# Kernel tuning notes

Measured on AMD Instinct MI355X. Metric: run time of the kernel, lower is better.

Reference implementation:

```python
import jax, jax.numpy as jnp
import numpy as np

N_NODES = 100000
N_EDGES = 1600000
D_IN = 256
N_HEADS = 4
D_OUT = 32
NEG_SLOPE = 0.2


def setup_inputs() -> dict:
    key = jax.random.key(0)
    k1, k2, k3, k4, k5, k6 = jax.random.split(key, 6)
    x = jax.random.normal(k1, (N_NODES, D_IN), dtype=jnp.float32)
    fc_w = jax.random.normal(k2, (N_HEADS * D_OUT, D_IN), dtype=jnp.float32) * (1.0 / np.sqrt(D_IN))
    attn_l = jax.random.normal(k3, (N_HEADS, D_OUT), dtype=jnp.float32) * 0.1
    attn_r = jax.random.normal(k4, (N_HEADS, D_OUT), dtype=jnp.float32) * 0.1
    src = jax.random.randint(k5, (N_EDGES,), 0, N_NODES, dtype=jnp.int64)
    dst = jax.random.randint(k6, (N_EDGES,), 0, N_NODES, dtype=jnp.int64)
    return {"x": x, "fc_w": fc_w, "attn_l": attn_l, "attn_r": attn_r, "src": src, "dst": dst}


def reference(x, fc_w, attn_l, attn_r, src, dst):
    N = x.shape[0]
    H, F = attn_l.shape
    # Linear projection: ft = fc(x) viewed as [N, H, F]
    ft = (x @ fc_w.T).reshape(N, H, F)
    # Per-node attention logits: el = <ft, a_l>, er = <ft, a_r>  -> [N, H]
    el = jnp.einsum("nhf,hf->nh", ft, attn_l)
    er = jnp.einsum("nhf,hf->nh", ft, attn_r)
    # Edge scores: e = leaky_relu(el[src] + er[dst])  -> [E, H]
    e = el[src] + er[dst]
    e = jnp.where(e > 0, e, NEG_SLOPE * e)
    # Segment (per-destination-node) softmax over incoming edges
    m = jax.ops.segment_max(e, dst, num_segments=N)  # [N, H]
    ex = jnp.exp(e - m[dst])                          # [E, H]
    denom = jax.ops.segment_sum(ex, dst, num_segments=N)  # [N, H]
    a = ex / denom[dst]                               # [E, H]
    # Weighted scatter-sum aggregation: out[n] = sum_{e: dst=n} a_e * ft[src_e]
    out = jax.ops.segment_sum(ft[src] * a[:, :, None], dst, num_segments=N)  # [N, H, F]
    return out
```

## Files before the change

kernel.cpp:

```cpp
#include <hip/hip_runtime.h>
#include <math.h>

#define N_NODES 100000
#define N_EDGES 1600000
#define D_IN 256
#define N_HEADS 4
#define D_OUT 32
#define D_HID 128
#define NEG_SLOPE 0.2f

#define BUCKET_SHIFT 8
#define BUCKET_NODES 256
#define NB ((N_NODES + BUCKET_NODES - 1) / BUCKET_NODES)
#define CAP 6144
#define TILE 2048
#define EPT 8
#define N_TILES ((N_EDGES + TILE - 1) / TILE)

typedef __attribute__((ext_vector_type(8))) short bf16x8;
typedef __attribute__((ext_vector_type(4))) float f32x4;

static __device__ __forceinline__ unsigned cvt2(float lo, float hi) {
  unsigned r;
  asm("v_cvt_pk_bf16_f32 %0, %1, %2" : "=v"(r) : "v"(lo), "v"(hi));
  return r;
}
static __device__ __forceinline__ float bfu_lo(unsigned u) {
  union { unsigned u; float f; } c; c.u = u << 16; return c.f;
}
static __device__ __forceinline__ float bfu_hi(unsigned u) {
  union { unsigned u; float f; } c; c.u = u & 0xFFFF0000u; return c.f;
}

#define LDA 40
__global__ __launch_bounds__(256) void k_gemm(const float* __restrict__ x,
                                              const float* __restrict__ w,
                                              unsigned short* __restrict__ ftb) {
  __shared__ short As[128 * LDA];
  __shared__ short Bs[128 * LDA];
  int t = threadIdx.x;
  int wave = t >> 6, lane = t & 63;
  int quad = lane >> 4, l16 = lane & 15;
  int rowBase = blockIdx.x * 128;
  int wm = (wave >> 1) * 64, wn = (wave & 1) * 64;
  f32x4 acc[4][4];
  #pragma unroll
  for (int mt = 0; mt < 4; ++mt)
    #pragma unroll
    for (int nt = 0; nt < 4; ++nt) {
      acc[mt][nt][0] = 0.f; acc[mt][nt][1] = 0.f;
      acc[mt][nt][2] = 0.f; acc[mt][nt][3] = 0.f;
    }

  for (int kb = 0; kb < D_IN; kb += 32) {
    #pragma unroll
    for (int p = 0; p < 4; ++p) {
      int idx = p * 256 + t;
      int r = idx >> 3;
      int kq = (idx & 7) * 4;
      int row = rowBase + r;
      float4 v = make_float4(0.f, 0.f, 0.f, 0.f);
      if (row < N_NODES) v = *(const float4*)&x[(size_t)row * D_IN + kb + kq];
      unsigned* d = (unsigned*)&As[r * LDA + kq];
      d[0] = cvt2(v.x, v.y);
      d[1] = cvt2(v.z, v.w);
    }
    #pragma unroll
    for (int p = 0; p < 4; ++p) {
      int idx = p * 256 + t;
      int r = idx >> 3;
      int kq = (idx & 7) * 4;
      float4 v = *(const float4*)&w[(size_t)r * D_IN + kb + kq];
      unsigned* d = (unsigned*)&Bs[r * LDA + kq];
      d[0] = cvt2(v.x, v.y);
      d[1] = cvt2(v.z, v.w);
    }
    __syncthreads();
    bf16x8 af[4], bfr[4];
    #pragma unroll
    for (int mt = 0; mt < 4; ++mt)
      af[mt] = *(const bf16x8*)&As[(wm + mt * 16 + l16) * LDA + quad * 8];
    #pragma unroll
    for (int nt = 0; nt < 4; ++nt)
      bfr[nt] = *(const bf16x8*)&Bs[(wn + nt * 16 + l16) * LDA + quad * 8];
    #pragma unroll
    for (int mt = 0; mt < 4; ++mt)
      #pragma unroll
      for (int nt = 0; nt < 4; ++nt)
        acc[mt][nt] = __builtin_amdgcn_mfma_f32_16x16x32_bf16(af[mt], bfr[nt], acc[mt][nt], 0, 0, 0);
    __syncthreads();
  }
  #pragma unroll
  for (int mt = 0; mt < 4; ++mt) {
    #pragma unroll
    for (int nt = 0; nt < 4; ++nt) {
      int col = wn + nt * 16 + l16;
      #pragma unroll
      for (int r = 0; r < 4; r += 2) {
        unsigned p = cvt2(acc[mt][nt][r], acc[mt][nt][r + 1]);
        int row = rowBase + wm + mt * 16 + quad * 4 + r;
        if (row < N_NODES)
          ftb[(size_t)row * D_HID + col] = (unsigned short)p;
        if (row + 1 < N_NODES)
          ftb[(size_t)(row + 1) * D_HID + col] = (unsigned short)(p >> 16);
      }
    }
  }
}

__global__ void k_eler(const unsigned short* __restrict__ ftb,
                       const float* __restrict__ al,
                       const float* __restrict__ ar,
                       float* __restrict__ el, float* __restrict__ er) {
  int gid = blockIdx.x * blockDim.x + threadIdx.x;
  if (gid >= N_NODES * N_HEADS) return;
  int n = gid >> 2, h = gid & 3;
  const unsigned* f = (const unsigned*)&ftb[(size_t)n * D_HID + h * D_OUT];
  const float* alh = &al[h * D_OUT];
  const float* arh = &ar[h * D_OUT];
  float sl = 0.f, sr = 0.f;
  #pragma unroll
  for (int i = 0; i < 16; ++i) {
    unsigned u = f[i];
    float lo = bfu_lo(u), hi = bfu_hi(u);
    sl += lo * alh[2 * i] + hi * alh[2 * i + 1];
    sr += lo * arh[2 * i] + hi * arh[2 * i + 1];
  }
  el[gid] = sl;
  er[gid] = sr;
}

__global__ __launch_bounds__(256) void k_bucket(const int* __restrict__ src,
                                                const int* __restrict__ dst,
                                                int* __restrict__ gfill,
                                                unsigned* __restrict__ pairs) {
  __shared__ int bcnt[NB];
  __shared__ int brsv[NB];
  __shared__ int brank[NB];
  int t = threadIdx.x;
  for (int tile = blockIdx.x; tile < N_TILES; tile += gridDim.x) {
    int e0 = tile * TILE + t * EPT;
    for (int i = t; i < NB; i += 256) { bcnt[i] = 0; brank[i] = 0; }
    __syncthreads();
    int ds[EPT], ss[EPT];
    if (e0 + EPT <= N_EDGES) {
      *(int4*)&ds[0] = *(const int4*)&dst[e0];
      *(int4*)&ds[4] = *(const int4*)&dst[e0 + 4];
      *(int4*)&ss[0] = *(const int4*)&src[e0];
      *(int4*)&ss[4] = *(const int4*)&src[e0 + 4];
    } else {
      #pragma unroll
      for (int k = 0; k < EPT; ++k) {
        int e = e0 + k;
        ds[k] = (e < N_EDGES) ? dst[e] : -1;
        ss[k] = (e < N_EDGES) ? src[e] : 0;
      }
    }
    #pragma unroll
    for (int k = 0; k < EPT; ++k)
      if (ds[k] >= 0) atomicAdd(&bcnt[ds[k] >> BUCKET_SHIFT], 1);
    __syncthreads();
    for (int i = t; i < NB; i += 256) {
      int c = bcnt[i];
      brsv[i] = (c > 0) ? atomicAdd(&gfill[i], c) : 0;
    }
    __syncthreads();
    #pragma unroll
    for (int k = 0; k < EPT; ++k) {
      if (ds[k] >= 0) {
        int b = ds[k] >> BUCKET_SHIFT;
        int r = brsv[b] + atomicAdd(&brank[b], 1);
        if (r < CAP)
          pairs[(size_t)b * CAP + r] =
              ((unsigned)ss[k] << 8) | (unsigned)(ds[k] & (BUCKET_NODES - 1));
      }
    }
    __syncthreads();
  }
}

__global__ __launch_bounds__(512) void k_scanbuckets(const int* __restrict__ gfill,
                                                     int* __restrict__ bbase,
                                                     int* __restrict__ offs) {
  __shared__ int ss[512];
  int t = threadIdx.x;
  int v = (t < NB) ? gfill[t] : 0;
  ss[t] = v;
  __syncthreads();
  #pragma unroll
  for (int d = 1; d < 512; d <<= 1) {
    int u = (t >= d) ? ss[t - d] : 0;
    __syncthreads();
    ss[t] += u;
    __syncthreads();
  }
  if (t < NB) bbase[t] = (t == 0) ? 0 : ss[t - 1];
  if (t == 0) offs[N_NODES] = N_EDGES;
}

__global__ __launch_bounds__(512) void k_localsort(const unsigned* __restrict__ pairs,
                                                   const int* __restrict__ gfill,
                                                   const int* __restrict__ bbase,
                                                   int* __restrict__ offs,
                                                   int* __restrict__ ssrc) {
  __shared__ int cnt_l[256];
  __shared__ int ss[256];
  __shared__ int cur_l[256];
  int b = blockIdx.x, t = threadIdx.x;
  int E = min(gfill[b], CAP);
  int base = bbase[b];
  const unsigned* pb = &pairs[(size_t)b * CAP];
  if (t < 256) cnt_l[t] = 0;
  __syncthreads();
  for (int i = t; i < E; i += 512)
    atomicAdd(&cnt_l[pb[i] & (BUCKET_NODES - 1)], 1);
  __syncthreads();
  if (t < 256) ss[t] = cnt_l[t];
  __syncthreads();
  #pragma unroll
  for (int d = 1; d < 256; d <<= 1) {
    int u = (t < 256 && t >= d) ? ss[t - d] : 0;
    __syncthreads();
    if (t < 256) ss[t] += u;
    __syncthreads();
  }
  if (t < 256) {
    int pre = (t == 0) ? 0 : ss[t - 1];
    int node = b * BUCKET_NODES + t;
    if (node < N_NODES) offs[node] = base + pre;
    cur_l[t] = pre;
  }
  __syncthreads();
  for (int i = t; i < E; i += 512) {
    unsigned p = pb[i];
    int pos = atomicAdd(&cur_l[p & (BUCKET_NODES - 1)], 1);
    ssrc[base + pos] = (int)(p >> 8);
  }
}

#define AHP 72
__global__ __launch_bounds__(256) void k_agg(const int* __restrict__ offs,
                                             const int* __restrict__ ssrc,
                                             const unsigned short* __restrict__ ftb,
                                             const float* __restrict__ el,
                                             const float* __restrict__ er,
                                             float* __restrict__ out) {
  __shared__ int   lds_s[4][64];
  __shared__ float lds_ah[4][4][AHP];
  int wave = threadIdx.x >> 6;
  int lane = threadIdx.x & 63;
  int n = blockIdx.x * 4 + wave;
  if (n >= N_NODES) return;
  int start = offs[n], end = offs[n + 1];
  int deg = end - start;

  if (deg <= 64) {
    float4 er4 = *(const float4*)&er[n * 4];
    bool valid = lane < deg;
    int s = valid ? ssrc[start + lane] : 0;
    float4 e4 = *(const float4*)&el[s * 4];
    float v[4] = {e4.x + er4.x, e4.y + er4.y, e4.z + er4.z, e4.w + er4.w};
    float m[4], ex[4], den[4];
    #pragma unroll
    for (int h = 0; h < 4; ++h) {
      v[h] = v[h] > 0.f ? v[h] : NEG_SLOPE * v[h];
      m[h] = valid ? v[h] : -INFINITY;
    }
    #pragma unroll
    for (int h = 0; h < 4; ++h)
      #pragma unroll
      for (int o = 32; o > 0; o >>= 1) m[h] = fmaxf(m[h], __shfl_xor(m[h], o));
    #pragma unroll
    for (int h = 0; h < 4; ++h) {
      ex[h] = valid ? __expf(v[h] - m[h]) : 0.f;
      den[h] = ex[h];
    }
    #pragma unroll
    for (int h = 0; h < 4; ++h)
      #pragma unroll
      for (int o = 32; o > 0; o >>= 1) den[h] += __shfl_xor(den[h], o);
    lds_s[wave][lane] = s;
    #pragma unroll
    for (int h = 0; h < 4; ++h)
      lds_ah[wave][h][lane] = ex[h] / den[h];
    __builtin_amdgcn_wave_barrier();

    int epar = lane >> 5;
    int c4 = (lane & 31) * 4;
    int hh = c4 >> 5;
    const unsigned short* fb = ftb + c4;
    float acc[4] = {0.f, 0.f, 0.f, 0.f};
    for (int j = 0; j < deg; j += 8) {
      int4   sv0 = *(const int4*)&lds_s[wave][j];
      int4   sv1 = *(const int4*)&lds_s[wave][j + 4];
      float4 av0 = *(const float4*)&lds_ah[wave][hh][j];
      float4 av1 = *(const float4*)&lds_ah[wave][hh][j + 4];
      int   sA = epar ? sv0.y : sv0.x;  float aA = epar ? av0.y : av0.x;
      int   sB = epar ? sv0.w : sv0.z;  float aB = epar ? av0.w : av0.z;
      int   sC = epar ? sv1.y : sv1.x;  float aC = epar ? av1.y : av1.x;
      int   sD = epar ? sv1.w : sv1.z;  float aD = epar ? av1.w : av1.z;
      uint2 uA = *(const uint2*)&fb[(size_t)sA * D_HID];
      uint2 uB = *(const uint2*)&fb[(size_t)sB * D_HID];
      uint2 uC = *(const uint2*)&fb[(size_t)sC * D_HID];
      uint2 uD = *(const uint2*)&fb[(size_t)sD * D_HID];
      acc[0] += aA * bfu_lo(uA.x); acc[1] += aA * bfu_hi(uA.x);
      acc[2] += aA * bfu_lo(uA.y); acc[3] += aA * bfu_hi(uA.y);
      acc[0] += aB * bfu_lo(uB.x); acc[1] += aB * bfu_hi(uB.x);
      acc[2] += aB * bfu_lo(uB.y); acc[3] += aB * bfu_hi(uB.y);
      acc[0] += aC * bfu_lo(uC.x); acc[1] += aC * bfu_hi(uC.x);
      acc[2] += aC * bfu_lo(uC.y); acc[3] += aC * bfu_hi(uC.y);
      acc[0] += aD * bfu_lo(uD.x); acc[1] += aD * bfu_hi(uD.x);
      acc[2] += aD * bfu_lo(uD.y); acc[3] += aD * bfu_hi(uD.y);
    }
    #pragma unroll
    for (int i = 0; i < 4; ++i) acc[i] += __shfl_xor(acc[i], 32);
    if (epar == 0)
      *(float4*)&out[(size_t)n * D_HID + c4] =
          make_float4(acc[0], acc[1], acc[2], acc[3]);
  } else {
    int f0 = lane * 2;
    int hh = lane >> 4;
    float2 acc = {0.f, 0.f};
    float4 er4 = *(const float4*)&er[n * 4];
    float erh[4] = {er4.x, er4.y, er4.z, er4.w};
    float m[4] = {-INFINITY, -INFINITY, -INFINITY, -INFINITY};
    for (int c = start; c < end; c += 64) {
      int i = c + lane;
      bool valid = i < end;
      int s = valid ? ssrc[i] : 0;
      float4 e4 = *(const float4*)&el[s * 4];
      float ee[4] = {e4.x, e4.y, e4.z, e4.w};
      #pragma unroll
      for (int h = 0; h < 4; ++h) {
        float v = ee[h] + erh[h];
        v = v > 0.f ? v : NEG_SLOPE * v;
        if (!valid) v = -INFINITY;
        m[h] = fmaxf(m[h], v);
      }
    }
    #pragma unroll
    for (int h = 0; h < 4; ++h)
      #pragma unroll
      for (int o = 32; o > 0; o >>= 1) m[h] = fmaxf(m[h], __shfl_xor(m[h], o));
    float den[4] = {0.f, 0.f, 0.f, 0.f};
    for (int c = start; c < end; c += 64) {
      int i = c + lane;
      bool valid = i < end;
      int s = valid ? ssrc[i] : 0;
      float4 e4 = *(const float4*)&el[s * 4];
      float ee[4] = {e4.x, e4.y, e4.z, e4.w};
      #pragma unroll
      for (int h = 0; h < 4; ++h) {
        float v = ee[h] + erh[h];
        v = v > 0.f ? v : NEG_SLOPE * v;
        den[h] += valid ? __expf(v - m[h]) : 0.f;
      }
    }
    #pragma unroll
    for (int h = 0; h < 4; ++h)
      #pragma unroll
      for (int o = 32; o > 0; o >>= 1) den[h] += __shfl_xor(den[h], o);
    float invd = 1.f / den[hh];
    for (int c = start; c < end; c += 64) {
      int i = c + lane;
      bool valid = i < end;
      int s = valid ? ssrc[i] : 0;
      float4 e4 = *(const float4*)&el[s * 4];
      float ee[4] = {e4.x, e4.y, e4.z, e4.w};
      float ex[4];
      #pragma unroll
      for (int h = 0; h < 4; ++h) {
        float v = ee[h] + erh[h];
        v = v > 0.f ? v : NEG_SLOPE * v;
        ex[h] = __expf(v - m[h]);
      }
      int cnt2 = min(64, end - c);
      for (int j = 0; j < cnt2; ++j) {
        int sj = __shfl(s, j);
        float a0 = __shfl(ex[0], j);
        float a1 = __shfl(ex[1], j);
        float a2 = __shfl(ex[2], j);
        float a3 = __shfl(ex[3], j);
        float ah = hh == 0 ? a0 : (hh == 1 ? a1 : (hh == 2 ? a2 : a3));
        ah *= invd;
        unsigned u = *(const unsigned*)&ftb[(size_t)sj * D_HID + f0];
        acc.x += ah * bfu_lo(u);
        acc.y += ah * bfu_hi(u);
      }
    }
    *(float2*)&out[(size_t)n * D_HID + f0] = acc;
  }
}

extern "C" void kernel_launch(void* const* d_in, const int* in_sizes, int n_in,
                              void* d_out, int out_size, void* d_ws, size_t ws_size,
                              hipStream_t stream) {
  const float* x      = (const float*)d_in[0];
  const float* fc_w   = (const float*)d_in[1];
  const float* attn_l = (const float*)d_in[2];
  const float* attn_r = (const float*)d_in[3];
  const int*   src    = (const int*)d_in[4];
  const int*   dst    = (const int*)d_in[5];
  float* out = (float*)d_out;

  char* wsp = (char*)d_ws;
  size_t off = 0;
  auto alloc = [&](size_t bytes) {
    void* p = wsp + off;
    off = (off + bytes + 255) & ~(size_t)255;
    return p;
  };
  unsigned short* ftb = (unsigned short*)alloc((size_t)N_NODES * D_HID * 2);
  float* el     = (float*)alloc((size_t)N_NODES * 4 * 4);
  float* er     = (float*)alloc((size_t)N_NODES * 4 * 4);
  int*   offs   = (int*)alloc((size_t)(N_NODES + 1) * 4);
  int*   ssrc   = (int*)alloc((size_t)N_EDGES * 4);
  int*   gfill  = (int*)alloc((size_t)NB * 4);
  int*   bbase  = (int*)alloc((size_t)NB * 4);
  unsigned* pairs = (unsigned*)alloc((size_t)NB * CAP * 4);

  hipMemsetAsync(gfill, 0, (size_t)NB * 4, stream);
  k_gemm<<<(N_NODES + 127) / 128, 256, 0, stream>>>(x, fc_w, ftb);
  k_eler<<<(N_NODES * N_HEADS + 255) / 256, 256, 0, stream>>>(ftb, attn_l, attn_r, el, er);
  k_bucket<<<N_TILES, 256, 0, stream>>>(src, dst, gfill, pairs);
  k_scanbuckets<<<1, 512, 0, stream>>>(gfill, bbase, offs);
  k_localsort<<<NB, 512, 0, stream>>>(pairs, gfill, bbase, offs, ssrc);
  k_agg<<<(N_NODES + 3) / 4, 256, 0, stream>>>(offs, ssrc, ftb, el, er, out);
}
```

Baseline: 324.7 us.

## Fuse el/er into GEMM epilogue, fold bucket scan into localsort, half-wave aggregation

Computes the per-node attention logits el/er directly from the fp32 MFMA accumulators in the GEMM epilogue using 16-lane shuffle reductions, which removes the separate k_eler kernel and its re-read of the bf16 features. The single-block bucket scan kernel is dropped; each localsort block now sums the fill counts of the preceding buckets itself. The aggregation kernel now assigns one node per half-wave (32 lanes, 4 features each), staging neighbor ids and attention weights in LDS for both low- and high-degree paths. This cuts kernel launches and idle lanes for typical degree ~16, at the cost of more shuffles in the GEMM epilogue and redundant prefix sums across localsort blocks.

```diff
diff --git a/kernel.cpp b/kernel.cpp
--- a/kernel.cpp
+++ b/kernel.cpp
@@ -35,7 +35,11 @@
 #define LDA 40
 __global__ __launch_bounds__(256) void k_gemm(const float* __restrict__ x,
                                               const float* __restrict__ w,
-                                              unsigned short* __restrict__ ftb) {
+                                              const float* __restrict__ al,
+                                              const float* __restrict__ ar,
+                                              unsigned short* __restrict__ ftb,
+                                              float* __restrict__ el,
+                                              float* __restrict__ er) {
   __shared__ short As[128 * LDA];
   __shared__ short Bs[128 * LDA];
   int t = threadIdx.x;
@@ -90,6 +94,7 @@
         acc[mt][nt] = __builtin_amdgcn_mfma_f32_16x16x32_bf16(af[mt], bfr[nt], acc[mt][nt], 0, 0, 0);
     __syncthreads();
   }
+
   #pragma unroll
   for (int mt = 0; mt < 4; ++mt) {
     #pragma unroll
@@ -106,38 +111,48 @@
       }
     }
   }
-}
-
-__global__ void k_eler(const unsigned short* __restrict__ ftb,
-                       const float* __restrict__ al,
-                       const float* __restrict__ ar,
-                       float* __restrict__ el, float* __restrict__ er) {
-  int gid = blockIdx.x * blockDim.x + threadIdx.x;
-  if (gid >= N_NODES * N_HEADS) return;
-  int n = gid >> 2, h = gid & 3;
-  const unsigned* f = (const unsigned*)&ftb[(size_t)n * D_HID + h * D_OUT];
-  const float* alh = &al[h * D_OUT];
-  const float* arh = &ar[h * D_OUT];
-  float sl = 0.f, sr = 0.f;
+
+  float alf[4], arf[4];
   #pragma unroll
-  for (int i = 0; i < 16; ++i) {
-    unsigned u = f[i];
-    float lo = bfu_lo(u), hi = bfu_hi(u);
-    sl += lo * alh[2 * i] + hi * alh[2 * i + 1];
-    sr += lo * arh[2 * i] + hi * arh[2 * i + 1];
-  }
-  el[gid] = sl;
-  er[gid] = sr;
+  for (int q = 0; q < 4; ++q) {
+    alf[q] = al[wn + q * 16 + l16];
+    arf[q] = ar[wn + q * 16 + l16];
+  }
+  int h0 = wn >> 5;
+  #pragma unroll
+  for (int mt = 0; mt < 4; ++mt) {
+    #pragma unroll
+    for (int r = 0; r < 4; ++r) {
+      float sl0 = acc[mt][0][r] * alf[0] + acc[mt][1][r] * alf[1];
+      float sl1 = acc[mt][2][r] * alf[2] + acc[mt][3][r] * alf[3];
+      float sr0 = acc[mt][0][r] * arf[0] + acc[mt][1][r] * arf[1];
+      float sr1 = acc[mt][2][r] * arf[2] + acc[mt][3][r] * arf[3];
+      #pragma unroll
+      for (int o = 1; o < 16; o <<= 1) {
+        sl0 += __shfl_xor(sl0, o);
+        sl1 += __shfl_xor(sl1, o);
+        sr0 += __shfl_xor(sr0, o);
+        sr1 += __shfl_xor(sr1, o);
+      }
+      int row = rowBase + wm + mt * 16 + quad * 4 + r;
+      if (l16 == 0 && row < N_NODES) {
+        *(float2*)&el[row * 4 + h0] = make_float2(sl0, sl1);
+        *(float2*)&er[row * 4 + h0] = make_float2(sr0, sr1);
+      }
+    }
+  }
 }
 
 __global__ __launch_bounds__(256) void k_bucket(const int* __restrict__ src,
                                                 const int* __restrict__ dst,
                                                 int* __restrict__ gfill,
-                                                unsigned* __restrict__ pairs) {
+                                                unsigned* __restrict__ pairs,
+                                                int* __restrict__ offs) {
   __shared__ int bcnt[NB];
   __shared__ int brsv[NB];
   __shared__ int brank[NB];
   int t = threadIdx.x;
+  if (blockIdx.x == 0 && t == 0) offs[N_NODES] = N_EDGES;
   for (int tile = blockIdx.x; tile < N_TILES; tile += gridDim.x) {
     int e0 = tile * TILE + t * EPT;
     for (int i = t; i < NB; i += 256) { bcnt[i] = 0; brank[i] = 0; }
@@ -179,39 +194,34 @@
   }
 }
 
-__global__ __launch_bounds__(512) void k_scanbuckets(const int* __restrict__ gfill,
-                                                     int* __restrict__ bbase,
-                                                     int* __restrict__ offs) {
-  __shared__ int ss[512];
-  int t = threadIdx.x;
-  int v = (t < NB) ? gfill[t] : 0;
-  ss[t] = v;
-  __syncthreads();
-  #pragma unroll
-  for (int d = 1; d < 512; d <<= 1) {
-    int u = (t >= d) ? ss[t - d] : 0;
-    __syncthreads();
-    ss[t] += u;
-    __syncthreads();
-  }
-  if (t < NB) bbase[t] = (t == 0) ? 0 : ss[t - 1];
-  if (t == 0) offs[N_NODES] = N_EDGES;
-}
-
 __global__ __launch_bounds__(512) void k_localsort(const unsigned* __restrict__ pairs,
                                                    const int* __restrict__ gfill,
-                                                   const int* __restrict__ bbase,
                                                    int* __restrict__ offs,
                                                    int* __restrict__ ssrc) {
   __shared__ int cnt_l[256];
   __shared__ int ss[256];
   __shared__ int cur_l[256];
+  __shared__ int redsum[8];
+  __shared__ int s_base;
   int b = blockIdx.x, t = threadIdx.x;
-  int E = min(gfill[b], CAP);
-  int base = bbase[b];
-  const unsigned* pb = &pairs[(size_t)b * CAP];
+  {
+    int v = (t < NB && t < b) ? gfill[t] : 0;
+    #pragma unroll
+    for (int o = 32; o > 0; o >>= 1) v += __shfl_xor(v, o);
+    if ((t & 63) == 0) redsum[t >> 6] = v;
+  }
   if (t < 256) cnt_l[t] = 0;
   __syncthreads();
+  if (t == 0) {
+    int s = 0;
+    #pragma unroll
+    for (int i = 0; i < 8; ++i) s += redsum[i];
+    s_base = s;
+  }
+  int E = min(gfill[b], CAP);
+  const unsigned* pb = &pairs[(size_t)b * CAP];
+  __syncthreads();
+  int base = s_base;
   for (int i = t; i < E; i += 512)
     atomicAdd(&cnt_l[pb[i] & (BUCKET_NODES - 1)], 1);
   __syncthreads();
@@ -238,26 +248,37 @@
   }
 }
 
-#define AHP 72
+#define AH_PAD 36
 __global__ __launch_bounds__(256) void k_agg(const int* __restrict__ offs,
                                              const int* __restrict__ ssrc,
                                              const unsigned short* __restrict__ ftb,
                                              const float* __restrict__ el,
                                              const float* __restrict__ er,
                                              float* __restrict__ out) {
-  __shared__ int   lds_s[4][64];
-  __shared__ float lds_ah[4][4][AHP];
+  __shared__ int   lds_s[4][2][32];
+  __shared__ float lds_ah[4][2][4][AH_PAD];
   int wave = threadIdx.x >> 6;
   int lane = threadIdx.x & 63;
-  int n = blockIdx.x * 4 + wave;
+  int half = lane >> 5;
+  int l32 = lane & 31;
+  int n = blockIdx.x * 8 + wave * 2 + half;
   if (n >= N_NODES) return;
   int start = offs[n], end = offs[n + 1];
   int deg = end - start;
 
-  if (deg <= 64) {
-    float4 er4 = *(const float4*)&er[n * 4];
-    bool valid = lane < deg;
-    int s = valid ? ssrc[start + lane] : 0;
+  int* sS = lds_s[wave][half];
+  float (*sA)[AH_PAD] = lds_ah[wave][half];
+
+  int c4 = l32 * 4;
+  int hh = l32 >> 3;
+  const unsigned short* fb = ftb + c4;
+  float a0 = 0.f, a1 = 0.f, a2 = 0.f, a3 = 0.f;
+
+  float4 er4 = *(const float4*)&er[n * 4];
+
+  if (deg <= 32) {
+    bool valid = l32 < deg;
+    int s = valid ? ssrc[start + l32] : 0;
     float4 e4 = *(const float4*)&el[s * 4];
     float v[4] = {e4.x + er4.x, e4.y + er4.y, e4.z + er4.z, e4.w + er4.w};
     float m[4], ex[4], den[4];
@@ -269,7 +290,7 @@
     #pragma unroll
     for (int h = 0; h < 4; ++h)
       #pragma unroll
-      for (int o = 32; o > 0; o >>= 1) m[h] = fmaxf(m[h], __shfl_xor(m[h], o));
+      for (int o = 16; o > 0; o >>= 1) m[h] = fmaxf(m[h], __shfl_xor(m[h], o));
     #pragma unroll
     for (int h = 0; h < 4; ++h) {
       ex[h] = valid ? __expf(v[h] - m[h]) : 0.f;
@@ -278,54 +299,32 @@
     #pragma unroll
     for (int h = 0; h < 4; ++h)
       #pragma unroll
-      for (int o = 32; o > 0; o >>= 1) den[h] += __shfl_xor(den[h], o);
-    lds_s[wave][lane] = s;
-    #pragma unroll
-    for (int h = 0; h < 4; ++h)
-      lds_ah[wave][h][lane] = ex[h] / den[h];
+      for (int o = 16; o > 0; o >>= 1) den[h] += __shfl_xor(den[h], o);
+    sS[l32] = s;
+    #pragma unroll
+    for (int h = 0; h < 4; ++h) sA[h][l32] = ex[h] / den[h];
     __builtin_amdgcn_wave_barrier();
-
-    int epar = lane >> 5;
-    int c4 = (lane & 31) * 4;
-    int hh = c4 >> 5;
-    const unsigned short* fb = ftb + c4;
-    float acc[4] = {0.f, 0.f, 0.f, 0.f};
-    for (int j = 0; j < deg; j += 8) {
-      int4   sv0 = *(const int4*)&lds_s[wave][j];
-      int4   sv1 = *(const int4*)&lds_s[wave][j + 4];
-      float4 av0 = *(const float4*)&lds_ah[wave][hh][j];
-      float4 av1 = *(const float4*)&lds_ah[wave][hh][j + 4];
-      int   sA = epar ? sv0.y : sv0.x;  float aA = epar ? av0.y : av0.x;
-      int   sB = epar ? sv0.w : sv0.z;  float aB = epar ? av0.w : av0.z;
-      int   sC = epar ? sv1.y : sv1.x;  float aC = epar ? av1.y : av1.x;
-      int   sD = epar ? sv1.w : sv1.z;  float aD = epar ? av1.w : av1.z;
-      uint2 uA = *(const uint2*)&fb[(size_t)sA * D_HID];
-      uint2 uB = *(const uint2*)&fb[(size_t)sB * D_HID];
-      uint2 uC = *(const uint2*)&fb[(size_t)sC * D_HID];
-      uint2 uD = *(const uint2*)&fb[(size_t)sD * D_HID];
-      acc[0] += aA * bfu_lo(uA.x); acc[1] += aA * bfu_hi(uA.x);
-      acc[2] += aA * bfu_lo(uA.y); acc[3] += aA * bfu_hi(uA.y);
-      acc[0] += aB * bfu_lo(uB.x); acc[1] += aB * bfu_hi(uB.x);
-      acc[2] += aB * bfu_lo(uB.y); acc[3] += aB * bfu_hi(uB.y);
-      acc[0] += aC * bfu_lo(uC.x); acc[1] += aC * bfu_hi(uC.x);
-      acc[2] += aC * bfu_lo(uC.y); acc[3] += aC * bfu_hi(uC.y);
-      acc[0] += aD * bfu_lo(uD.x); acc[1] += aD * bfu_hi(uD.x);
-      acc[2] += aD * bfu_lo(uD.y); acc[3] += aD * bfu_hi(uD.y);
-    }
-    #pragma unroll
-    for (int i = 0; i < 4; ++i) acc[i] += __shfl_xor(acc[i], 32);
-    if (epar == 0)
-      *(float4*)&out[(size_t)n * D_HID + c4] =
-          make_float4(acc[0], acc[1], acc[2], acc[3]);
+    for (int j = 0; j < deg; j += 4) {
+      int4   sv = *(const int4*)&sS[j];
+      float4 av = *(const float4*)&sA[hh][j];
+      uint2 uA = *(const uint2*)&fb[(size_t)sv.x * D_HID];
+      uint2 uB = *(const uint2*)&fb[(size_t)sv.y * D_HID];
+      uint2 uC = *(const uint2*)&fb[(size_t)sv.z * D_HID];
+      uint2 uD = *(const uint2*)&fb[(size_t)sv.w * D_HID];
+      a0 += av.x * bfu_lo(uA.x); a1 += av.x * bfu_hi(uA.x);
+      a2 += av.x * bfu_lo(uA.y); a3 += av.x * bfu_hi(uA.y);
+      a0 += av.y * bfu_lo(uB.x); a1 += av.y * bfu_hi(uB.x);
+      a2 += av.y * bfu_lo(uB.y); a3 += av.y * bfu_hi(uB.y);
+      a0 += av.z * bfu_lo(uC.x); a1 += av.z * bfu_hi(uC.x);
+      a2 += av.z * bfu_lo(uC.y); a3 += av.z * bfu_hi(uC.y);
+      a0 += av.w * bfu_lo(uD.x); a1 += av.w * bfu_hi(uD.x);
+      a2 += av.w * bfu_lo(uD.y); a3 += av.w * bfu_hi(uD.y);
+    }
   } else {
-    int f0 = lane * 2;
-    int hh = lane >> 4;
-    float2 acc = {0.f, 0.f};
-    float4 er4 = *(const float4*)&er[n * 4];
     float erh[4] = {er4.x, er4.y, er4.z, er4.w};
     float m[4] = {-INFINITY, -INFINITY, -INFINITY, -INFINITY};
-    for (int c = start; c < end; c += 64) {
-      int i = c + lane;
+    for (int c = start; c < end; c += 32) {
+      int i = c + l32;
       bool valid = i < end;
       int s = valid ? ssrc[i] : 0;
       float4 e4 = *(const float4*)&el[s * 4];
@@ -334,17 +333,16 @@
       for (int h = 0; h < 4; ++h) {
         float v = ee[h] + erh[h];
         v = v > 0.f ? v : NEG_SLOPE * v;
-        if (!valid) v = -INFINITY;
-        m[h] = fmaxf(m[h], v);
+        m[h] = fmaxf(m[h], valid ? v : -INFINITY);
       }
     }
     #pragma unroll
     for (int h = 0; h < 4; ++h)
       #pragma unroll
-      for (int o = 32; o > 0; o >>= 1) m[h] = fmaxf(m[h], __shfl_xor(m[h], o));
+      for (int o = 16; o > 0; o >>= 1) m[h] = fmaxf(m[h], __shfl_xor(m[h], o));
     float den[4] = {0.f, 0.f, 0.f, 0.f};
-    for (int c = start; c < end; c += 64) {
-      int i = c + lane;
+    for (int c = start; c < end; c += 32) {
+      int i = c + l32;
       bool valid = i < end;
       int s = valid ? ssrc[i] : 0;
       float4 e4 = *(const float4*)&el[s * 4];
@@ -359,37 +357,48 @@
     #pragma unroll
     for (int h = 0; h < 4; ++h)
       #pragma unroll
-      for (int o = 32; o > 0; o >>= 1) den[h] += __shfl_xor(den[h], o);
-    float invd = 1.f / den[hh];
-    for (int c = start; c < end; c += 64) {
-      int i = c + lane;
+      for (int o = 16; o > 0; o >>= 1) den[h] += __shfl_xor(den[h], o);
+    float invd[4];
+    #pragma unroll
+    for (int h = 0; h < 4; ++h) invd[h] = 1.f / den[h];
+    for (int c = start; c < end; c += 32) {
+      int i = c + l32;
       bool valid = i < end;
       int s = valid ? ssrc[i] : 0;
       float4 e4 = *(const float4*)&el[s * 4];
       float ee[4] = {e4.x, e4.y, e4.z, e4.w};
-      float ex[4];
+      float av[4];
       #pragma unroll
       for (int h = 0; h < 4; ++h) {
         float v = ee[h] + erh[h];
         v = v > 0.f ? v : NEG_SLOPE * v;
-        ex[h] = __expf(v - m[h]);
-      }
-      int cnt2 = min(64, end - c);
-      for (int j = 0; j < cnt2; ++j) {
-        int sj = __shfl(s, j);
-        float a0 = __shfl(ex[0], j);
-        float a1 = __shfl(ex[1], j);
-        float a2 = __shfl(ex[2], j);
-        float a3 = __shfl(ex[3], j);
-        float ah = hh == 0 ? a0 : (hh == 1 ? a1 : (hh == 2 ? a2 : a3));
-        ah *= invd;
-        unsigned u = *(const unsigned*)&ftb[(size_t)sj * D_HID + f0];
-        acc.x += ah * bfu_lo(u);
-        acc.y += ah * bfu_hi(u);
-      }
-    }
-    *(float2*)&out[(size_t)n * D_HID + f0] = acc;
-  }
+        av[h] = valid ? __expf(v - m[h]) * invd[h] : 0.f;
+      }
+      __builtin_amdgcn_wave_barrier();
+      sS[l32] = s;
+      #pragma unroll
+      for (int h = 0; h < 4; ++h) sA[h][l32] = av[h];
+      __builtin_amdgcn_wave_barrier();
+      int cnt = min(32, end - c);
+      for (int j = 0; j < cnt; j += 4) {
+        int4   sv = *(const int4*)&sS[j];
+        float4 aw = *(const float4*)&sA[hh][j];
+        uint2 uA = *(const uint2*)&fb[(size_t)sv.x * D_HID];
+        uint2 uB = *(const uint2*)&fb[(size_t)sv.y * D_HID];
+        uint2 uC = *(const uint2*)&fb[(size_t)sv.z * D_HID];
+        uint2 uD = *(const uint2*)&fb[(size_t)sv.w * D_HID];
+        a0 += aw.x * bfu_lo(uA.x); a1 += aw.x * bfu_hi(uA.x);
+        a2 += aw.x * bfu_lo(uA.y); a3 += aw.x * bfu_hi(uA.y);
+        a0 += aw.y * bfu_lo(uB.x); a1 += aw.y * bfu_hi(uB.x);
+        a2 += aw.y * bfu_lo(uB.y); a3 += aw.y * bfu_hi(uB.y);
+        a0 += aw.z * bfu_lo(uC.x); a1 += aw.z * bfu_hi(uC.x);
+        a2 += aw.z * bfu_lo(uC.y); a3 += aw.z * bfu_hi(uC.y);
+        a0 += aw.w * bfu_lo(uD.x); a1 += aw.w * bfu_hi(uD.x);
+        a2 += aw.w * bfu_lo(uD.y); a3 += aw.w * bfu_hi(uD.y);
+      }
+    }
+  }
+  *(float4*)&out[(size_t)n * D_HID + c4] = make_float4(a0, a1, a2, a3);
 }
 
 extern "C" void kernel_launch(void* const* d_in, const int* in_sizes, int n_in,
@@ -416,14 +425,11 @@
   int*   offs   = (int*)alloc((size_t)(N_NODES + 1) * 4);
   int*   ssrc   = (int*)alloc((size_t)N_EDGES * 4);
   int*   gfill  = (int*)alloc((size_t)NB * 4);
-  int*   bbase  = (int*)alloc((size_t)NB * 4);
   unsigned* pairs = (unsigned*)alloc((size_t)NB * CAP * 4);
 
   hipMemsetAsync(gfill, 0, (size_t)NB * 4, stream);
-  k_gemm<<<(N_NODES + 127) / 128, 256, 0, stream>>>(x, fc_w, ftb);
-  k_eler<<<(N_NODES * N_HEADS + 255) / 256, 256, 0, stream>>>(ftb, attn_l, attn_r, el, er);
-  k_bucket<<<N_TILES, 256, 0, stream>>>(src, dst, gfill, pairs);
-  k_scanbuckets<<<1, 512, 0, stream>>>(gfill, bbase, offs);
-  k_localsort<<<NB, 512, 0, stream>>>(pairs, gfill, bbase, offs, ssrc);
-  k_agg<<<(N_NODES + 3) / 4, 256, 0, stream>>>(offs, ssrc, ftb, el, er, out);
-}
+  k_gemm<<<(N_NODES + 127) / 128, 256, 0, stream>>>(x, fc_w, attn_l, attn_r, ftb, el, er);
+  k_bucket<<<N_TILES, 256, 0, stream>>>(src, dst, gfill, pairs, offs);
+  k_localsort<<<NB, 512, 0, stream>>>(pairs, gfill, offs, ssrc);
+  k_agg<<<(N_NODES + 7) / 8, 256, 0, stream>>>(offs, ssrc, ftb, el, er, out);
+}
```

Result: slower. 331.4 us (+2.1%).
